# Performance work log

Measured on AMD Instinct MI355X. Metric: run time of the kernel, lower is better.

Reference implementation:

```python
import jax, jax.numpy as jnp
import numpy as np

EPS = 1e-15

def _sqn(x):
    return jnp.sum(x * x, axis=-1, keepdims=True)

def _nrm(x):
    return jnp.sqrt(jnp.clip(_sqn(x), EPS))

def artanh(x):
    return jnp.arctanh(jnp.clip(x, -1 + 1e-7, 1 - 1e-7))

def project(x):
    n = _nrm(x)
    mx = 1.0 - 1e-5
    return jnp.where(n > mx, x / n * mx, x)

def mobius_add(x, y):
    x2, y2 = _sqn(x), _sqn(y)
    xy = jnp.sum(x * y, -1, keepdims=True)
    num = (1 + 2 * xy + y2) * x + (1 - x2) * y
    den = 1 + 2 * xy + x2 * y2
    return num / jnp.clip(den, EPS)

def expmap0(u):
    n = _nrm(u)
    return project(jnp.tanh(n) * u / n)

def logmap0(x):
    n = _nrm(x)
    return artanh(n) * x / n

def pdist(x, y):
    return 2.0 * artanh(_nrm(mobius_add(-x, y)))[..., 0]

def mobius_matvec(x, W):
    # x [..., din], W [din, dout]
    xn = _nrm(x)
    mx = x @ W
    mxn = _nrm(mx)
    return project(jnp.tanh(mxn / xn * artanh(xn)) * mx / mxn)

def mobius_pw_mul(w, x):
    xn = _nrm(x)
    wx = w * x
    wxn = _nrm(wx)
    return project(jnp.tanh(wxn / xn * artanh(xn)) * wx / wxn)

def mobius_linear(x, W, b, nonlin=None):
    out = project(mobius_add(mobius_matvec(x, W), b))
    if nonlin is not None:
        out = project(expmap0(nonlin(logmap0(out))))
    return out

def poincare_to_klein(x):
    return 2 * x / (1 + _sqn(x))

def klein_to_poincare(k):
    return k / (1 + jnp.sqrt(jnp.clip(1 - _sqn(k), EPS)))

def weighted_mobius_midpoint(values, weights):
    # values [..., L, d], weights [..., L, 1]; gyromidpoint via Klein model
    kl = poincare_to_klein(values)
    gamma = 1.0 / jnp.sqrt(jnp.clip(1 - _sqn(kl), EPS))
    num = jnp.sum(weights * gamma * kl, axis=-2)
    den = jnp.sum(weights * gamma, axis=-2)
    return klein_to_poincare(num / jnp.clip(den, EPS))

def mobius_gru(x_seq, Wih, Whh, bias):
    # x_seq [L,B,din]; Wih [3H,din]; Whh [3H,H]; bias [3,H] (points on ball)
    H = Whh.shape[1]
    W_ir, W_ihh, W_iz = jnp.split(Wih, 3, axis=0)
    W_hr, W_hhh, W_hz = jnp.split(Whh, 3, axis=0)
    b_r, b_h, b_z = bias[0], bias[1], bias[2]
    def one_tf(W, h, U, x, b):
        return mobius_add(mobius_add(mobius_matvec(h, W.T), mobius_matvec(x, U.T)), b)
    def step(h, x):
        z = jax.nn.sigmoid(logmap0(one_tf(W_hz, h, W_iz, x, b_z)))
        r = jax.nn.sigmoid(logmap0(one_tf(W_hr, h, W_ir, x, b_r)))
        rh = mobius_pw_mul(r, h)
        h_tilde = one_tf(W_hhh, rh, W_ihh, x, b_h)
        delta = mobius_add(-h, h_tilde)
        hn = mobius_add(h, mobius_pw_mul(z, delta))
        return hn, hn
    h0 = jnp.zeros((x_seq.shape[1], H), x_seq.dtype)
    return jax.lax.scan(step, h0, x_seq)[1]  # [L,B,H]

def mobius_rnn(x_seq, W, U, b):
    # x_seq [L,B,d]; W [d,d] hidden->hidden, U [d,d] input->hidden
    def step(h, x):
        hn = project(mobius_add(mobius_add(mobius_matvec(h, W), mobius_matvec(x, U)), b))
        return hn, hn
    h0 = jnp.zeros(x_seq.shape[1:], x_seq.dtype)
    return jax.lax.scan(step, h0, x_seq)[1]

def distance_attention(values, pos_idx, pos_embeds, Wq, bq, Wk, bk, beta):
    # values [B,L,d], pos_idx [B,L] int
    pe = pos_embeds[pos_idx]
    attn_emb = mobius_add(values, pe)
    q = mobius_linear(attn_emb, Wq, bq)
    k = mobius_linear(attn_emb, Wk, bk)
    d = pdist(q, k)                      # [B,L]
    w = jax.nn.softmax(-beta * d, axis=1)
    return weighted_mobius_midpoint(values, w[..., None]), w

def _forward(context, ctx_position, mentions, mention_chars,
             word_lut, char_lut,
             gru_f_Wih, gru_f_Whh, gru_f_b, gru_b_Wih, gru_b_Whh, gru_b_b,
             w2s_W, w2s_b,
             men_pos, men_Wq, men_bq, men_Wk, men_bk, men_beta,
             char_W, char_U, char_b,
             cc_Wa, cc_Wb, cc_bias,
             ctx_pos, ctx_Wq, ctx_bq, ctx_Wk, ctx_bk, ctx_beta,
             fc_Wm, fc_Wc, fc_Wch, fc_bias,
             mlr_p, mlr_a):
    # ---- mention encoder ----
    men_emb = word_lut[mentions]                                   # B x ML x E
    mv = mobius_linear(men_emb, w2s_W, w2s_b, nonlin=jnp.tanh)     # B x ML x 2S
    ML = mentions.shape[1]
    pos_idx = jnp.where(mentions > 0, jnp.arange(1, ML + 1)[None, :], 0)
    mention_vec, _ = distance_attention(mv, pos_idx, men_pos, men_Wq, men_bq, men_Wk, men_bk, men_beta)
    ch = char_lut[mention_chars]                                   # B x CL x S
    char_states = mobius_rnn(ch.transpose(1, 0, 2), char_W, char_U, char_b).transpose(1, 0, 2)
    char_vec = weighted_mobius_midpoint(char_states, jnp.ones_like(char_states[..., :1]))
    # ---- context encoder (bi-directional hyperbolic GRU) ----
    fwd_emb = word_lut[context].transpose(1, 0, 2)                 # L x B x E
    bkwd_emb = word_lut[context[:, ::-1]].transpose(1, 0, 2)
    fwd_states = mobius_gru(fwd_emb, gru_f_Wih, gru_f_Whh, gru_f_b).transpose(1, 0, 2)
    bkwd_states = mobius_gru(bkwd_emb, gru_b_Wih, gru_b_Whh, gru_b_b).transpose(1, 0, 2)[:, ::-1]
    # ---- mobius concat of directions ----
    ctx = project(mobius_add(mobius_add(mobius_matvec(fwd_states, cc_Wa), mobius_matvec(bkwd_states, cc_Wb)), cc_bias))
    ctx_vec, _ = distance_attention(ctx, ctx_position, ctx_pos, ctx_Wq, ctx_bq, ctx_Wk, ctx_bk, ctx_beta)
    # ---- full mobius concat ----
    joint = mobius_add(mobius_matvec(mention_vec, fc_Wm), mobius_matvec(ctx_vec, fc_Wc))
    joint = project(mobius_add(mobius_add(joint, mobius_matvec(char_vec, fc_Wch)), fc_bias))
    # ---- hyperbolic MLR ----
    z = mobius_add(-mlr_p[None], joint[:, None])                   # B x C x D
    a_n = jnp.sqrt(jnp.clip(jnp.sum(mlr_a * mlr_a, -1), EPS))      # C
    num = 2 * jnp.einsum('bcd,cd->bc', z, mlr_a)
    den = jnp.clip(1 - jnp.sum(z * z, -1), EPS) * a_n
    return 2 * a_n * jnp.arcsinh(num / den)                        # B x C

def setup_inputs() -> dict:
    key = jax.random.key(0)
    ks = iter(jax.random.split(key, 64))
    B, L, ML, CL = 256, 128, 8, 16
    V, CV, E, S, C = 50000, 128, 300, 256, 128
    S2, D = 2 * 256, 5 * 256
    POS_CTX = 2 * 64 + 2  # context_len*2+2
    def u(k, shape, a):
        return jax.random.uniform(k, shape, jnp.float32, -a, a)
    def ball(k, shape, a=1e-4):
        return expmap0(u(k, shape, a))
    def wmat(k, din, dout):
        return u(k, (din, dout), 1.0 / np.sqrt(din))
    inp = {}
    inp['context'] = jax.random.randint(next(ks), (B, L), 0, V)
    inp['ctx_position'] = jax.random.randint(next(ks), (B, L), 0, POS_CTX)
    inp['mentions'] = jax.random.randint(next(ks), (B, ML), 0, V)
    inp['mention_chars'] = jax.random.randint(next(ks), (B, CL), 0, CV)
    inp['word_lut'] = ball(next(ks), (V, E))
    inp['char_lut'] = ball(next(ks), (CV, S))
    for pre in ('gru_f', 'gru_b'):
        inp[pre + '_Wih'] = u(next(ks), (3 * S, E), 1.0 / np.sqrt(S))
        inp[pre + '_Whh'] = u(next(ks), (3 * S, S), 1.0 / np.sqrt(S))
        inp[pre + '_b'] = ball(next(ks), (3, S))
    inp['w2s_W'] = wmat(next(ks), E, S2)
    inp['w2s_b'] = ball(next(ks), (S2,))
    inp['men_pos'] = ball(next(ks), (ML + 1, S2))
    inp['men_Wq'] = wmat(next(ks), S2, S2)
    inp['men_bq'] = ball(next(ks), (S2,))
    inp['men_Wk'] = wmat(next(ks), S2, S2)
    inp['men_bk'] = ball(next(ks), (S2,))
    inp['men_beta'] = u(next(ks), (1,), 0.01)
    inp['char_W'] = wmat(next(ks), S, S)
    inp['char_U'] = wmat(next(ks), S, S)
    inp['char_b'] = ball(next(ks), (S,))
    inp['cc_Wa'] = wmat(next(ks), S, S2)
    inp['cc_Wb'] = wmat(next(ks), S, S2)
    inp['cc_bias'] = ball(next(ks), (S2,))
    inp['ctx_pos'] = ball(next(ks), (POS_CTX, S2))
    inp['ctx_Wq'] = wmat(next(ks), S2, S2)
    inp['ctx_bq'] = ball(next(ks), (S2,))
    inp['ctx_Wk'] = wmat(next(ks), S2, S2)
    inp['ctx_bk'] = ball(next(ks), (S2,))
    inp['ctx_beta'] = u(next(ks), (1,), 0.01)
    inp['fc_Wm'] = wmat(next(ks), S2, D)
    inp['fc_Wc'] = wmat(next(ks), S2, D)
    inp['fc_Wch'] = wmat(next(ks), S, D)
    inp['fc_bias'] = ball(next(ks), (D,))
    inp['mlr_p'] = ball(next(ks), (C, D))
    inp['mlr_a'] = u(next(ks), (C, D), 1.0 / np.sqrt(D))
    return inp

def reference(context, ctx_position, mentions, mention_chars,
              word_lut, char_lut,
              gru_f_Wih, gru_f_Whh, gru_f_b, gru_b_Wih, gru_b_Whh, gru_b_b,
              w2s_W, w2s_b,
              men_pos, men_Wq, men_bq, men_Wk, men_bk, men_beta,
              char_W, char_U, char_b,
              cc_Wa, cc_Wb, cc_bias,
              ctx_pos, ctx_Wq, ctx_bq, ctx_Wk, ctx_bk, ctx_beta,
              fc_Wm, fc_Wc, fc_Wch, fc_bias,
              mlr_p, mlr_a):
    return _forward(context, ctx_position, mentions, mention_chars,
                    word_lut, char_lut,
                    gru_f_Wih, gru_f_Whh, gru_f_b, gru_b_Wih, gru_b_Whh, gru_b_b,
                    w2s_W, w2s_b,
                    men_pos, men_Wq, men_bq, men_Wk, men_bk, men_beta,
                    char_W, char_U, char_b,
                    cc_Wa, cc_Wb, cc_bias,
                    ctx_pos, ctx_Wq, ctx_bq, ctx_Wk, ctx_bk, ctx_beta,
                    fc_Wm, fc_Wc, fc_Wch, fc_bias,
                    mlr_p, mlr_a)
```

## Files before the change

### kernel.cpp

```cpp
#include <hip/hip_runtime.h>
#include <cstddef>
#include <cstdint>


#define EPS_  1e-15f
#define PMAX_ 0.99999f

typedef __attribute__((ext_vector_type(8))) short bf16x8;
typedef __attribute__((ext_vector_type(4))) float f32x4;
typedef __attribute__((ext_vector_type(8))) unsigned short us8;

__device__ __forceinline__ float wred(float v){
#pragma unroll
  for (int o = 32; o; o >>= 1) v += __shfl_xor(v, o, 64);
  return v;
}
__device__ __forceinline__ void wred2(float& a, float& b){
#pragma unroll
  for (int o = 32; o; o >>= 1){ a += __shfl_xor(a, o, 64); b += __shfl_xor(b, o, 64); }
}
__device__ __forceinline__ void wred3(float& a, float& b, float& c){
#pragma unroll
  for (int o = 32; o; o >>= 1){
    a += __shfl_xor(a, o, 64); b += __shfl_xor(b, o, 64); c += __shfl_xor(c, o, 64);
  }
}
__device__ __forceinline__ void wred4(float& a, float& b, float& c, float& d){
#pragma unroll
  for (int o = 32; o; o >>= 1){
    a += __shfl_xor(a, o, 64); b += __shfl_xor(b, o, 64);
    c += __shfl_xor(c, o, 64); d += __shfl_xor(d, o, 64);
  }
}
__device__ __forceinline__ float wredmax(float v){
#pragma unroll
  for (int o = 32; o; o >>= 1) v = fmaxf(v, __shfl_xor(v, o, 64));
  return v;
}
__device__ __forceinline__ float snorm(float s){ return sqrtf(fmaxf(s, EPS_)); }
__device__ __forceinline__ float clamp11(float x){
  return fminf(fmaxf(x, -1.f + 1e-7f), 1.f - 1e-7f);
}
__device__ __forceinline__ float bf2f(unsigned short u){
  union { unsigned int i; float f; } v; v.i = ((unsigned int)u) << 16; return v.f;
}
__device__ __forceinline__ unsigned short f2bf(float f){
  union { float f; unsigned int i; } v; v.f = f;
  unsigned int x = v.i;
  x += 0x7fffu + ((x >> 16) & 1u);
  return (unsigned short)(x >> 16);
}
__device__ __forceinline__ float bflo(unsigned u){
  union { unsigned i; float f; } v; v.i = u << 16; return v.f;
}
__device__ __forceinline__ float bfhi(unsigned u){
  union { unsigned i; float f; } v; v.i = u & 0xffff0000u; return v.f;
}

template<int N>
__device__ __forceinline__ float sq_part(const float* a){
  float s = 0.f;
#pragma unroll
  for (int i = 0; i < N; i++) s += a[i]*a[i];
  return s;
}
template<int N>
__device__ __forceinline__ float dot_part(const float* a, const float* b){
  float s = 0.f;
#pragma unroll
  for (int i = 0; i < N; i++) s += a[i]*b[i];
  return s;
}
template<int N>
__device__ __forceinline__ void madd_vec(const float* x, float x2, const float* y,
                                         float y2, float xy, float* o){
  const float c1 = 1.f + 2.f*xy + y2;
  const float c2 = 1.f - x2;
  const float inv = 1.f / fmaxf(1.f + 2.f*xy + x2*y2, EPS_);
#pragma unroll
  for (int i = 0; i < N; i++) o[i] = (c1*x[i] + c2*y[i]) * inv;
}
template<int N>
__device__ __forceinline__ void mt_project(float* v, float mxn2, float xn2, float* n2out){
  const float xn  = snorm(xn2);
  const float mxn = snorm(mxn2);
  const float t   = tanhf(mxn/xn * atanhf(clamp11(xn)));
  float sc = t/mxn;
  float n2 = sc*sc*mxn2;
  const float n = snorm(n2);
  if (n > PMAX_){ const float s = PMAX_/n; sc *= s; n2 *= s*s; }
#pragma unroll
  for (int i = 0; i < N; i++) v[i] *= sc;
  *n2out = n2;
// ... 165 lines not shown
      if (kb < K){
        const float4 f = *reinterpret_cast<const float4*>(Bm + (long)kb*N + n0 + bn);
        bv[0]=f.x; bv[1]=f.y; bv[2]=f.z; bv[3]=f.w;
      } else { bv[0]=bv[1]=bv[2]=bv[3]=0.f; }
    }
    __syncthreads();
    As[sk+0][sm]=av[0]; As[sk+1][sm]=av[1]; As[sk+2][sm]=av[2]; As[sk+3][sm]=av[3];
    *reinterpret_cast<float4*>(&Bs[bk][bn]) = make_float4(bv[0],bv[1],bv[2],bv[3]);
    __syncthreads();
#pragma unroll
    for (int k = 0; k < 8; k++){
      float a[8], bb[8];
      *(float4*)&a[0]  = *(const float4*)&As[k][tr*8];
      *(float4*)&a[4]  = *(const float4*)&As[k][tr*8+4];
      *(float4*)&bb[0] = *(const float4*)&Bs[k][tc*8];
      *(float4*)&bb[4] = *(const float4*)&Bs[k][tc*8+4];
#pragma unroll
      for (int i = 0; i < 8; i++)
#pragma unroll
        for (int j = 0; j < 8; j++) acc[i][j] += a[i]*bb[j];
    }
  }
#pragma unroll
  for (int i = 0; i < 8; i++){
    const long row = m0 + tr*8 + i;
    *(float4*)(Cm + row*N + n0 + tc*8)     = make_float4(acc[i][0],acc[i][1],acc[i][2],acc[i][3]);
    *(float4*)(Cm + row*N + n0 + tc*8 + 4) = make_float4(acc[i][4],acc[i][5],acc[i][6],acc[i][7]);
  }
}

__global__ __launch_bounds__(256) void transpose_k(const float* __restrict__ src,
    float* __restrict__ dst, int R, int Kc)
{
  __shared__ float t[32][33];
  const int bx = blockIdx.x * 32;
  const int by = blockIdx.y * 32;
  const int tx = threadIdx.x & 31, ty = threadIdx.x >> 5;
#pragma unroll
  for (int i = 0; i < 32; i += 8){
    const int j = by + ty + i, k = bx + tx;
    t[ty+i][tx] = (j < R && k < Kc) ? src[(long)j*Kc + k] : 0.f;
  }
  __syncthreads();
#pragma unroll
  for (int i = 0; i < 32; i += 8){
    const int k = bx + ty + i, j = by + tx;
    if (k < Kc && j < R) dst[(long)k*R + j] = t[tx][ty+i];
  }
}

__global__ __launch_bounds__(256) void packT16(const float* __restrict__ src,
    unsigned short* __restrict__ dst, int K, int N, int Kp)
{
  __shared__ float t[32][33];
  const int bx = blockIdx.x*32;
  const int by = blockIdx.y*32;
  const int tx = threadIdx.x & 31, ty = threadIdx.x >> 5;
#pragma unroll
  for (int i = 0; i < 32; i += 8){
    const int k = bx + ty + i, n = by + tx;
    t[ty+i][tx] = (k < K && n < N) ? src[(long)k*N + n] : 0.f;
  }
  __syncthreads();
#pragma unroll
  for (int i = 0; i < 32; i += 8){
    const int k = bx + tx, n = by + ty + i;
    if (k < Kp && n < N) dst[(long)n*Kp + k] = f2bf(t[tx][ty+i]);
  }
}

__global__ void pack_wih(const float* __restrict__ w0, const float* __restrict__ w1,
                         unsigned short* __restrict__ dst)
{
  const int tid = blockIdx.x*256 + threadIdx.x;
  if (tid < 2*768*320){
    const int d = tid / (768*320);
    const int rem = tid - d*768*320;
    const int n = rem / 320, k = rem - n*320;
    const float* src = d ? w1 : w0;
    dst[tid] = (k < 300) ? f2bf(src[n*300 + k]) : (unsigned short)0;
  }
}

__global__ void pack_whh16(const float* __restrict__ WtHH,
                           unsigned short* __restrict__ Wrz16,
                           unsigned short* __restrict__ Wh16)
{
  const int tid = blockIdx.x*256 + threadIdx.x;
  if (tid < 2*256*768){
    const int col = tid % 768, rk = tid / 768;
    const unsigned short v = f2bf(WtHH[tid]);
    if (col < 256)       Wrz16[(long)rk*512 + col] = v;
    else if (col < 512)  Wh16 [(long)rk*256 + (col - 256)] = v;
    else                 Wrz16[(long)rk*512 + 256 + (col - 512)] = v;
  }
}

__global__ void build_idx(const int* __restrict__ context, const int* __restrict__ mchars,
                          int* __restrict__ ctxidx, int* __restrict__ chidx)
{
  const int tid = blockIdx.x*256 + threadIdx.x;
  if (tid < 32768){
    const int t = tid >> 8, b = tid & 255;
    ctxidx[tid] = context[b*128 + t];
  } else if (tid < 32768 + 4096){
    const int o = tid - 32768;
    const int t = o >> 8, b = o & 255;
    chidx[o] = mchars[b*16 + t];
  }
}

__global__ __launch_bounds__(256) void sqn_gather(const float* __restrict__ lut,
    const int* __restrict__ idx, int K, float* __restrict__ outp)
{
  const int wv = threadIdx.x >> 6, lane = threadIdx.x & 63;
  const int r = blockIdx.x*4 + wv;
  const float* row = lut + (long)idx[r]*K;
  float s = 0.f;
  for (int k = lane; k < K; k += 64) s += row[k]*row[k];
  s = wred(s);
  if (lane == 0) outp[r] = s;
}

__global__ __launch_bounds__(256) void xg_transform(const float* __restrict__ mx,
    const float* __restrict__ xsqn, unsigned short* __restrict__ outp,
    float* __restrict__ n2o, int G)
{
  const int wv = threadIdx.x >> 6, lane = threadIdx.x & 63;
  const int wg = blockIdx.x*4 + wv;
  const int row = wg / G, g = wg - row*G;
  const long base = (long)row*(G*256) + g*256;
  float M[4];
#pragma unroll
  for (int i = 0; i < 4; i++) M[i] = mx[base + i*64 + lane];
  const float mxn2 = wred(sq_part<4>(M));
  float pn2; mt_project<4>(M, mxn2, xsqn[row], &pn2);
  float s = 0.f;
#pragma unroll
  for (int i = 0; i < 4; i++){
    const unsigned short u = f2bf(M[i]);
    outp[base + i*64 + lane] = u;
    const float rv = bf2f(u);
    s += rv*rv;
  }
  s = wred(s);
  if (lane == 0) n2o[wg] = s;
}

#define GRU_LDS_BYTES 153664

__global__ __launch_bounds__(512,1) void gru_kernel(
    const unsigned short* __restrict__ xg,
    const float* __restrict__ xgn2,
    const unsigned short* __restrict__ Wrz16,
    const unsigned short* __restrict__ Wh16,
    const float* __restrict__ bias_f, const float* __restrict__ bias_b,
    unsigned short* __restrict__ states_f, unsigned short* __restrict__ states_b)
{
  extern __shared__ __align__(16) char smem[];
  float* wbuf = (float*)smem;
  float* hs   = (float*)(smem + 131072);
  float* part = (float*)(smem + 133120);
  float* rhb  = (float*)(smem + 149504);
  float* zb   = (float*)(smem + 151552);
  float* scal = (float*)(smem + 153600);

  const int bid = blockIdx.x;
  const int dir = bid >> 7;
  const int brow0 = (bid & 127) * 2;
  const int tid = threadIdx.x;
  const int w = tid >> 6, lane = tid & 63;
  const int j0 = lane << 2;

  const unsigned short* xgd = xg + (long)dir*32768*768;
  const float* xnd = xgn2 + (long)dir*32768*3;
  const unsigned short* wrz_d = Wrz16 + (long)dir*256*512;
  const unsigned short* wh_d  = Wh16  + (long)dir*256*256;
  const float* bias = dir ? bias_b : bias_f;
  unsigned short* states = dir ? states_b : states_f;

  const int fg  = w & 1;
  const int kq4 = w >> 1;
  const int qk8 = w;
  const int crow  = (w >> 1) & 1;
  const int cgate = w & 1;

  float bg[4], bh4[4] = {0,0,0,0};
  float bg2, bh2 = 0.f;
#pragma unroll
  for (int i = 0; i < 4; i++) bg[i] = bias[(cgate ? 512 : 0) + j0 + i];
  bg2 = wred(sq_part<4>(bg));
  if (w < 2){
#pragma unroll
    for (int i = 0; i < 4; i++) bh4[i] = bias[256 + j0 + i];
    bh2 = wred(sq_part<4>(bh4));
  }

  float h[4] = {0.f,0.f,0.f,0.f};
  float hn2 = 0.f;
  if (w < 2){
#pragma unroll
    for (int i = 0; i < 4; i++) hs[w*256 + j0 + i] = 0.f;
    if (lane == 0){ scal[w*2 + 0] = 0.f; scal[w*2 + 1] = 0.f; }
  }

  int cb = 0;
  stage64k8(wrz_d, wbuf, w, lane);

  for (int t = 0; t < 128; t++){
    const int tt = dir ? (127 - t) : t;
    float xgv[4] = {0,0,0,0}, y2g = 0.f, xgh4[4] = {0,0,0,0}, y2h = 0.f;
    if (w < 4){
      const long rxg = (long)tt*256 + brow0 + crow;
      const ushort4 u = *(const ushort4*)(xgd + rxg*768 + (cgate ? 512 : 0) + j0);
      xgv[0]=bf2f(u.x); xgv[1]=bf2f(u.y); xgv[2]=bf2f(u.z); xgv[3]=bf2f(u.w);
      y2g = xnd[rxg*3 + (cgate ? 2 : 0)];
      if (w < 2){
        const long rxh = (long)tt*256 + brow0 + w;
        const ushort4 uh = *(const ushort4*)(xgd + rxh*768 + 256 + j0);
        xgh4[0]=bf2f(uh.x); xgh4[1]=bf2f(uh.y); xgh4[2]=bf2f(uh.z); xgh4[3]=bf2f(uh.w);
        y2h = xnd[rxh*3 + 1];
      }
    }

    float s00=0.f,s01=0.f,s02=0.f,s03=0.f, s10=0.f,s11=0.f,s12=0.f,s13=0.f;
#pragma unroll 1
    for (int c = 0; c < 4; c++){
      __syncthreads();
      if (c < 3) stage64k8((const char*)wrz_d + (size_t)(c+1)*65536,
                           wbuf + (cb^1)*16384, w, lane);
      const uint2* wb2 = (const uint2*)(wbuf + cb*16384);
      const int kb = c*64 + kq4*16;
#pragma unroll
      for (int kk = 0; kk < 4; kk++){
        const float4 hb0 = *(const float4*)&hs[0*256 + kb + kk*4];
        const float4 hb1 = *(const float4*)&hs[1*256 + kb + kk*4];
#pragma unroll
        for (int q = 0; q < 4; q++){
          const uint2 wvv = wb2[(kq4*16 + kk*4 + q)*128 + fg*64 + lane];
          const float w0 = bflo(wvv.x), w1 = bfhi(wvv.x);
          const float w2 = bflo(wvv.y), w3 = bfhi(wvv.y);
          const float h0 = (&hb0.x)[q], h1 = (&hb1.x)[q];
          s00 += h0*w0; s01 += h0*w1; s02 += h0*w2; s03 += h0*w3;
          s10 += h1*w0; s11 += h1*w1; s12 += h1*w2; s13 += h1*w3;
        }
      }
      cb ^= 1;
    }
    {
      float* p1 = part + kq4*1024 + fg*256 + j0;
      *(float4*)p1         = make_float4(s00,s01,s02,s03);
      *(float4*)(p1 + 512) = make_float4(s10,s11,s12,s13);
    }
    __syncthreads();
    stage64k8(wh_d, wbuf + (cb^1)*16384, w, lane);
    cb ^= 1;

    if (w < 4){
      const float* pa = part + crow*512 + cgate*256 + j0;
      const float4 a0 = *(const float4*)pa;
      const float4 a1 = *(const float4*)(pa + 1024);
      const float4 a2 = *(const float4*)(pa + 2048);
      const float4 a3 = *(const float4*)(pa + 3072);
      float a[4] = { (a0.x+a1.x)+(a2.x+a3.x), (a0.y+a1.y)+(a2.y+a3.y),
                     (a0.z+a1.z)+(a2.z+a3.z), (a0.w+a1.w)+(a2.w+a3.w) };
      const float hn2v = scal[crow*2 + 0];
      const float xn_h = snorm(hn2v), art_h = atanhf(clamp11(xn_h));
      const float p2 = wred(sq_part<4>(a));
      float sc, n2; mt_scale(p2, xn_h, art_h, &sc, &n2);
#pragma unroll
      for (int i = 0; i < 4; i++) a[i] *= sc;
      const float xy = wred(dot_part<4>(a, xgv));
      float m1[4]; madd_vec<4>(a, n2, xgv, y2g, xy, m1);
      float m1n2 = sq_part<4>(m1), xyb = dot_part<4>(m1, bg);
      wred2(m1n2, xyb);
      float m2[4]; madd_vec<4>(m1, m1n2, bg, bg2, xyb, m2);
      const float m2n2 = wred(sq_part<4>(m2));
      const float nn = snorm(m2n2), fgc = atanhf(clamp11(nn))/nn;
      float g4[4];
#pragma unroll
      for (int i = 0; i < 4; i++) g4[i] = 1.f/(1.f + expf(-fgc*m2[i]));
      if (cgate == 0){
        float h4[4];
        *(float4*)h4 = *(const float4*)&hs[crow*256 + j0];
        float rh[4]; float wx2 = 0.f;
#pragma unroll
        for (int i = 0; i < 4; i++){ rh[i] = g4[i]*h4[i]; wx2 += rh[i]*rh[i]; }
        wx2 = wred(wx2);
        float rhn2, scrh;
        {
          const float wxn = snorm(wx2);
          const float trh = tanhf(wxn/xn_h * art_h);
          scrh = trh/wxn; rhn2 = trh*trh;
          const float n = snorm(rhn2);
          if (n > PMAX_){ const float f = PMAX_/n; scrh *= f; rhn2 *= f*f; }
        }
#pragma unroll
        for (int i = 0; i < 4; i++) rh[i] *= scrh;
        *(float4*)&rhb[crow*256 + j0] = make_float4(rh[0],rh[1],rh[2],rh[3]);
        if (lane == 0) scal[crow*2 + 1] = rhn2;
      } else {
        *(float4*)&zb[crow*256 + j0] = make_float4(g4[0],g4[1],g4[2],g4[3]);
      }
    }

    float r00=0.f,r01=0.f,r02=0.f,r03=0.f, r10=0.f,r11=0.f,r12=0.f,r13=0.f;
#pragma unroll 1
    for (int c = 0; c < 2; c++){
      __syncthreads();
      if (c < 1) stage64k8((const char*)wh_d + 65536, wbuf + (cb^1)*16384, w, lane);
      const uint2* wb2 = (const uint2*)(wbuf + cb*16384);
      const int kb = c*128 + qk8*16;
#pragma unroll
      for (int kk = 0; kk < 4; kk++){
        const float4 hb0 = *(const float4*)&rhb[0*256 + kb + kk*4];
        const float4 hb1 = *(const float4*)&rhb[1*256 + kb + kk*4];
#pragma unroll
        for (int q = 0; q < 4; q++){
          const uint2 wvv = wb2[(qk8*16 + kk*4 + q)*64 + lane];
          const float w0 = bflo(wvv.x), w1 = bfhi(wvv.x);
          const float w2 = bflo(wvv.y), w3 = bfhi(wvv.y);
          const float h0 = (&hb0.x)[q], h1 = (&hb1.x)[q];
          r00 += h0*w0; r01 += h0*w1; r02 += h0*w2; r03 += h0*w3;
          r10 += h1*w0; r11 += h1*w1; r12 += h1*w2; r13 += h1*w3;
        }
      }
      cb ^= 1;
    }
    {
      float* p2 = part + qk8*512 + j0;
      *(float4*)p2         = make_float4(r00,r01,r02,r03);
      *(float4*)(p2 + 256) = make_float4(r10,r11,r12,r13);
    }
    __syncthreads();
    if (t < 127){
      stage64k8(wrz_d, wbuf + (cb^1)*16384, w, lane);
      cb ^= 1;
    }

    if (w < 2){
      float ah[4];
      {
        float4 p[8];
#pragma unroll
        for (int q = 0; q < 8; q++)
          p[q] = *(const float4*)(part + q*512 + w*256 + j0);
        ah[0] = ((p[0].x+p[1].x)+(p[2].x+p[3].x)) + ((p[4].x+p[5].x)+(p[6].x+p[7].x));
        ah[1] = ((p[0].y+p[1].y)+(p[2].y+p[3].y)) + ((p[4].y+p[5].y)+(p[6].y+p[7].y));
        ah[2] = ((p[0].z+p[1].z)+(p[2].z+p[3].z)) + ((p[4].z+p[5].z)+(p[6].z+p[7].z));
        ah[3] = ((p[0].w+p[1].w)+(p[2].w+p[3].w)) + ((p[4].w+p[5].w)+(p[6].w+p[7].w));
      }
      const float rhn2v = scal[w*2 + 1];
      const float rxn = snorm(rhn2v), artr = atanhf(clamp11(rxn));
      float mx2 = sq_part<4>(ah), xyraw = dot_part<4>(ah, xgh4);
      wred2(mx2, xyraw);
      float sch, pn2; mt_scale(mx2, rxn, artr, &sch, &pn2);
#pragma unroll
      for (int i = 0; i < 4; i++) ah[i] *= sch;
      const float xy = xyraw * sch;
      float m1[4]; madd_vec<4>(ah, pn2, xgh4, y2h, xy, m1);
      float m1n2 = sq_part<4>(m1), xyb = dot_part<4>(m1, bh4);
      wred2(m1n2, xyb);
      float ht[4]; madd_vec<4>(m1, m1n2, bh4, bh2, xyb, ht);
      float htn2 = sq_part<4>(ht);
      float nh[4];
#pragma unroll
      for (int i = 0; i < 4; i++) nh[i] = -h[i];
      float xyd = dot_part<4>(nh, ht);
      wred2(htn2, xyd);
      float dl[4]; madd_vec<4>(nh, hn2, ht, htn2, xyd, dl);
      float z4[4];
      *(float4*)z4 = *(const float4*)&zb[w*256 + j0];
      float pw[4]; float dln2 = 0.f, wz2 = 0.f, xyhr = 0.f;
#pragma unroll
      for (int i = 0; i < 4; i++){
        dln2 += dl[i]*dl[i];
        pw[i] = z4[i]*dl[i];
        wz2  += pw[i]*pw[i];
        xyhr += h[i]*pw[i];
      }
      wred3(dln2, wz2, xyhr);
      float pwn2, scpw;
      {
        const float dn   = snorm(dln2);
        const float artd = atanhf(clamp11(dn));
        const float wzn  = snorm(wz2);
        const float tpw  = tanhf(wzn/dn * artd);
        scpw = tpw/wzn; pwn2 = tpw*tpw;
        const float n = snorm(pwn2);
        if (n > PMAX_){ const float f = PMAX_/n; scpw *= f; pwn2 *= f*f; }
      }
#pragma unroll
      for (int i = 0; i < 4; i++) pw[i] *= scpw;
      const float xyh = xyhr * scpw;
      float hnew[4]; madd_vec<4>(h, hn2, pw, pwn2, xyh, hnew);
#pragma unroll
      for (int i = 0; i < 4; i++) h[i] = hnew[i];
      hn2 = wred(sq_part<4>(h));
      *(float4*)&hs[w*256 + j0] = make_float4(h[0],h[1],h[2],h[3]);
      if (lane == 0) scal[w*2 + 0] = hn2;
      unsigned short* srow = states + ((long)(brow0 + w)*128 + tt)*256 + j0;
      ushort4 su; su.x=f2bf(h[0]); su.y=f2bf(h[1]); su.z=f2bf(h[2]); su.w=f2bf(h[3]);
      *(ushort4*)srow = su;
    }
  }
}

__global__ __launch_bounds__(256) void char_rnn(
    const unsigned short* __restrict__ xgc,
    const float* __restrict__ Wc,
    const float* __restrict__ cb,
    float* __restrict__ cstates)
{
  const int wv = threadIdx.x >> 6, lane = threadIdx.x & 63;
  const int b = blockIdx.x*4 + wv;
  const int j0 = lane << 2;
  __shared__ __align__(16) float hs[4][256];
  float h[4] = {0.f,0.f,0.f,0.f};
  float hn2 = 0.f;
#pragma unroll
  for (int i = 0; i < 4; i++) hs[wv][j0+i] = 0.f;
  float cbv[4];
#pragma unroll
  for (int i = 0; i < 4; i++) cbv[i] = cb[j0+i];
  const float cb2 = wred(sq_part<4>(cbv));
  for (int t = 0; t < 16; t++){
    __syncthreads();
    const unsigned short* xr = xgc + ((long)t*256 + b)*256;
    float xgv[4];
    { const ushort4 u = *(const ushort4*)(xr + j0); xgv[0]=bf2f(u.x); xgv[1]=bf2f(u.y); xgv[2]=bf2f(u.z); xgv[3]=bf2f(u.w); }
    float a[4]={0.f,0.f,0.f,0.f};
#pragma unroll 2
    for (int k0 = 0; k0 < 256; k0 += 4){
      const float4 hk = *(const float4*)&hs[wv][k0];
#pragma unroll
      for (int kk = 0; kk < 4; kk++){
        const float hv = (&hk.x)[kk];
        const float4 w4 = *(const float4*)(Wc + (long)(k0+kk)*256 + j0);
        a[0] += hv*w4.x; a[1] += hv*w4.y; a[2] += hv*w4.z; a[3] += hv*w4.w;
      }
    }
    const float mxn2 = wred(sq_part<4>(a));
    float pn2; mt_project<4>(a, mxn2, hn2, &pn2);
    const float y2 = wred(sq_part<4>(xgv));
    const float xy = wred(dot_part<4>(a, xgv));
    float m1[4]; madd_vec<4>(a, pn2, xgv, y2, xy, m1);
    const float m1n2 = wred(sq_part<4>(m1));
    const float xyb  = wred(dot_part<4>(m1, cbv));
    float m2[4]; madd_vec<4>(m1, m1n2, cbv, cb2, xyb, m2);
    float m2n2 = wred(sq_part<4>(m2));
    project_vec<4>(m2, &m2n2);
#pragma unroll
    for (int i = 0; i < 4; i++) h[i] = m2[i];
    hn2 = m2n2;
    *(float4*)&hs[wv][j0] = make_float4(h[0],h[1],h[2],h[3]);
    *(float4*)(cstates + ((long)b*16 + t)*256 + j0) = make_float4(h[0],h[1],h[2],h[3]);
  }
}

__global__ __launch_bounds__(256) void cc_rowwise(const unsigned short* __restrict__ sf,
    const unsigned short* __restrict__ sb, const float* __restrict__ mxa,
    const float* __restrict__ mxb, const float* __restrict__ ccb,
    unsigned short* __restrict__ ctxo, int rowoff)
{
  const int wv = threadIdx.x >> 6, lane = threadIdx.x & 63;
  const int rloc = blockIdx.x*4 + wv;
  const long r = rowoff + rloc;
  float s = 0.f;
#pragma unroll
  for (int i = 0; i < 4; i++){ const float v = bf2f(sf[r*256 + i*64+lane]); s += v*v; }
  const float sfn2 = wred(s);
  s = 0.f;
#pragma unroll
  for (int i = 0; i < 4; i++){ const float v = bf2f(sb[r*256 + i*64+lane]); s += v*v; }
  const float sbn2 = wred(s);
  float A[8], Bv[8];
#pragma unroll
  for (int i = 0; i < 8; i++){ A[i]  = mxa[(long)rloc*512 + i*64+lane];
                               Bv[i] = mxb[(long)rloc*512 + i*64+lane]; }
  float pan2, pbn2;
  { const float n2 = wred(sq_part<8>(A));  mt_project<8>(A,  n2, sfn2, &pan2); }
  { const float n2 = wred(sq_part<8>(Bv)); mt_project<8>(Bv, n2, sbn2, &pbn2); }
// ... 332 lines not shown

__global__ __launch_bounds__(256) void mlr_kernel(const float* __restrict__ joint,
    const float* __restrict__ P, const float* __restrict__ A, float* __restrict__ outp)
{
  const int wv = threadIdx.x >> 6, lane = threadIdx.x & 63;
  const int pair = blockIdx.x*4 + wv;
  const long b = pair >> 7, c = pair & 127;
  float Pv[20], J[20];
#pragma unroll
  for (int i = 0; i < 20; i++){
    Pv[i] = -P[c*1280 + i*64+lane];
    J[i]  = joint[b*1280 + i*64+lane];
  }
  const float p2 = wred(sq_part<20>(Pv));
  const float j2 = wred(sq_part<20>(J));
  const float xy = wred(dot_part<20>(Pv, J));
  float Z[20]; madd_vec<20>(Pv, p2, J, j2, xy, Z);
  float sza = 0.f, sz2 = 0.f, sa2 = 0.f;
#pragma unroll
  for (int i = 0; i < 20; i++){
    const float a = A[c*1280 + i*64+lane];
    sza += Z[i]*a; sz2 += Z[i]*Z[i]; sa2 += a*a;
  }
  float za = sza, z2 = sz2, a2 = sa2;
  wred3(za, z2, a2);
  const float an = sqrtf(fmaxf(a2, EPS_));
  const float v = 2.f*za / (fmaxf(1.f - z2, EPS_)*an);
  if (lane == 0) outp[pair] = 2.f*an*asinhf(v);
}

extern "C" void kernel_launch(void* const* d_in, const int* in_sizes, int n_in,
                              void* d_out, int out_size, void* d_ws, size_t ws_size,
                              hipStream_t stream)
{
  (void)in_sizes; (void)n_in; (void)out_size;
  const int*   context   = (const int*)  d_in[0];
  const int*   ctx_position=(const int*) d_in[1];
  const int*   mentions  = (const int*)  d_in[2];
  const int*   mchars    = (const int*)  d_in[3];
  const float* word_lut  = (const float*)d_in[4];
  const float* char_lut  = (const float*)d_in[5];
  const float* gf_Wih    = (const float*)d_in[6];
  const float* gf_Whh    = (const float*)d_in[7];
  const float* gf_b      = (const float*)d_in[8];
  const float* gb_Wih    = (const float*)d_in[9];
  const float* gb_Whh    = (const float*)d_in[10];
  const float* gb_b      = (const float*)d_in[11];
  const float* w2s_W     = (const float*)d_in[12];
  const float* w2s_b     = (const float*)d_in[13];
  const float* men_pos   = (const float*)d_in[14];
  const float* men_Wq    = (const float*)d_in[15];
  const float* men_bq    = (const float*)d_in[16];
  const float* men_Wk    = (const float*)d_in[17];
  const float* men_bk    = (const float*)d_in[18];
  const float* men_beta  = (const float*)d_in[19];
  const float* char_W    = (const float*)d_in[20];
  const float* char_U    = (const float*)d_in[21];
  const float* char_b    = (const float*)d_in[22];
  const float* cc_Wa     = (const float*)d_in[23];
  const float* cc_Wb     = (const float*)d_in[24];
  const float* cc_bias   = (const float*)d_in[25];
  const float* ctx_pos_t = (const float*)d_in[26];
  const float* ctx_Wq    = (const float*)d_in[27];
  const float* ctx_bq    = (const float*)d_in[28];
  const float* ctx_Wk    = (const float*)d_in[29];
  const float* ctx_bk    = (const float*)d_in[30];
  const float* ctx_beta  = (const float*)d_in[31];
  const float* fc_Wm     = (const float*)d_in[32];
  const float* fc_Wc     = (const float*)d_in[33];
  const float* fc_Wch    = (const float*)d_in[34];
  const float* fc_bias   = (const float*)d_in[35];
  const float* mlr_p     = (const float*)d_in[36];
  const float* mlr_a     = (const float*)d_in[37];
  float* out = (float*)d_out;

  char* wsb = (char*)d_ws;
  size_t off = 0;
  auto alloc = [&](size_t bytes) -> void* {
    void* p = wsb + off;
    off += (bytes + 255) & ~(size_t)255;
    return p;
  };
  float* WtHH = (float*)alloc(2UL*256*768*4);
  unsigned short* Wrz16 = (unsigned short*)alloc(2UL*256*512*2);
  unsigned short* Wh16  = (unsigned short*)alloc(2UL*256*256*2);
  unsigned short* WihP  = (unsigned short*)alloc(2UL*768*320*2);
  unsigned short* ctxWqP= (unsigned short*)alloc(512UL*512*2);
  unsigned short* ctxWkP= (unsigned short*)alloc(512UL*512*2);
  unsigned short* ccWaP = (unsigned short*)alloc(512UL*256*2);
  unsigned short* ccWbP = (unsigned short*)alloc(512UL*256*2);
  unsigned short* menWqP= (unsigned short*)alloc(512UL*512*2);
  unsigned short* menWkP= (unsigned short*)alloc(512UL*512*2);
  unsigned short* w2sP  = (unsigned short*)alloc(512UL*320*2);
  unsigned short* charUP= (unsigned short*)alloc(256UL*256*2);
  int*   ctxidx = (int*)alloc(32768UL*4);
  int*   chidx  = (int*)alloc(4096UL*4);
  float* xsqn   = (float*)alloc(32768UL*4);
  float* msqn   = (float*)alloc(2048UL*4);
  float* chsqn  = (float*)alloc(4096UL*4);
  unsigned short* xg = (unsigned short*)alloc(2UL*32768*768*2);
  float* xgn2 = (float*)alloc(2UL*32768*3*4);
  float* chn2d = (float*)alloc(4096UL*4);
  unsigned short* states_f = (unsigned short*)alloc(32768UL*256*2);
  unsigned short* states_b = (unsigned short*)alloc(32768UL*256*2);
  unsigned short* ctxv = (unsigned short*)alloc(32768UL*512*2);
  float* attn_sqn = (float*)alloc(32768UL*4);
  float* dctx = (float*)alloc(32768UL*4);
  float* wctx = (float*)alloc(32768UL*4);
  float* ctx_vec = (float*)alloc(256UL*512*4);
  float* mxbuf = (float*)alloc(2UL*8192*512*4);
  float* mv = (float*)alloc(2048UL*512*4);
  unsigned short* attn_embm = (unsigned short*)alloc(2048UL*512*2);
  float* amsqn = (float*)alloc(2048UL*4);
  float* dm = (float*)alloc(2048UL*4);
  float* wm = (float*)alloc(2048UL*4);
  float* mention_vec = (float*)alloc(256UL*512*4);
  unsigned short* xgc = (unsigned short*)alloc(4096UL*256*2);
  float* char_states = (float*)alloc(4096UL*256*4);
  float* char_vec = (float*)alloc(256UL*256*4);
  float* joint = (float*)alloc(256UL*1280*4);
  if (off > ws_size) return;
  unsigned short* attn_embc = xg;
  float* mxh0 = mxbuf;
  float* mxh1 = mxbuf + 8192UL*512;

  transpose_k<<<dim3(8,24), 256,0,stream>>>(gf_Whh, WtHH,            768, 256);
  transpose_k<<<dim3(8,24), 256,0,stream>>>(gb_Whh, WtHH + 256*768,  768, 256);
  pack_whh16<<<1536,256,0,stream>>>(WtHH, Wrz16, Wh16);
  pack_wih<<<1920,256,0,stream>>>(gf_Wih, gb_Wih, WihP);
  packT16<<<dim3(16,16),256,0,stream>>>(ctx_Wq, ctxWqP, 512, 512, 512);
  packT16<<<dim3(16,16),256,0,stream>>>(ctx_Wk, ctxWkP, 512, 512, 512);
  packT16<<<dim3(8,16), 256,0,stream>>>(cc_Wa,  ccWaP,  256, 512, 256);
  packT16<<<dim3(8,16), 256,0,stream>>>(cc_Wb,  ccWbP,  256, 512, 256);
  packT16<<<dim3(16,16),256,0,stream>>>(men_Wq, menWqP, 512, 512, 512);
  packT16<<<dim3(16,16),256,0,stream>>>(men_Wk, menWkP, 512, 512, 512);
  packT16<<<dim3(10,16),256,0,stream>>>(w2s_W,  w2sP,   300, 512, 320);
  packT16<<<dim3(8,8),  256,0,stream>>>(char_U, charUP, 256, 256, 256);

  build_idx<<<144,256,0,stream>>>(context, mchars, ctxidx, chidx);
  sqn_gather<<<8192,256,0,stream>>>(word_lut, ctxidx, 300, xsqn);
  sqn_gather<<<512, 256,0,stream>>>(word_lut, mentions, 300, msqn);
  sqn_gather<<<1024,256,0,stream>>>(char_lut, chidx, 256, chsqn);

  for (int d2 = 0; d2 < 2; d2++){
    const unsigned short* wihp = WihP + (size_t)d2*768*320;
    for (int c = 0; c < 4; c++){
      mfma_mm<1><<<dim3(6,128),256,0,stream>>>(word_lut, ctxidx + c*8192, wihp,
                                               mxbuf, 8192, 768, 300, 320);
      xg_transform<<<6144,256,0,stream>>>(mxbuf, xsqn + c*8192,
          xg + ((size_t)d2*32768 + (size_t)c*8192)*768,
          xgn2 + ((size_t)d2*32768 + (size_t)c*8192)*3, 3);
    }
  }

  (void)hipFuncSetAttribute((const void*)gru_kernel,
      hipFuncAttributeMaxDynamicSharedMemorySize, GRU_LDS_BYTES);
  gru_kernel<<<256,512,GRU_LDS_BYTES,stream>>>(xg, xgn2, Wrz16, Wh16,
                                               gf_b, gb_b, states_f, states_b);

  for (int c = 0; c < 4; c++){
    mfma_mm<2><<<dim3(4,128),256,0,stream>>>(states_f + (size_t)c*8192*256, nullptr,
                                             ccWaP, mxh0, 8192, 512, 256, 256);
    mfma_mm<2><<<dim3(4,128),256,0,stream>>>(states_b + (size_t)c*8192*256, nullptr,
                                             ccWbP, mxh1, 8192, 512, 256, 256);
    cc_rowwise<<<2048,256,0,stream>>>(states_f, states_b, mxh0, mxh1, cc_bias,
                                      ctxv, c*8192);
  }

  attn_add<<<8192,256,0,stream>>>(ctxv, ctx_position, ctx_pos_t, attn_embc, attn_sqn);
  for (int c = 0; c < 4; c++){
    mfma_mm<2><<<dim3(4,128),256,0,stream>>>(attn_embc + (size_t)c*8192*512, nullptr,
                                             ctxWqP, mxh0, 8192, 512, 512, 512);
    mfma_mm<2><<<dim3(4,128),256,0,stream>>>(attn_embc + (size_t)c*8192*512, nullptr,
                                             ctxWkP, mxh1, 8192, 512, 512, 512);
    qk_pdist<<<2048,256,0,stream>>>(mxh0, mxh1, attn_sqn + c*8192, ctx_bq, ctx_bk,
                                    dctx + c*8192);
  }
  softmax128<<<64,256,0,stream>>>(dctx, ctx_beta, wctx);
  midpoint_wide<<<256,512,0,stream>>>(ctxv, wctx, ctx_vec);

  mfma_mm<1><<<dim3(4,32),256,0,stream>>>(word_lut, mentions, w2sP, mxh0,
                                          2048, 512, 300, 320);
  mv_rowwise<<<512,256,0,stream>>>(mxh0, msqn, w2s_b, mv);
  attn_add_m<<<512,256,0,stream>>>(mv, mentions, men_pos, attn_embm, amsqn);
  mfma_mm<2><<<dim3(4,32),256,0,stream>>>(attn_embm, nullptr, menWqP, mxh0,
                                          2048, 512, 512, 512);
  mfma_mm<2><<<dim3(4,32),256,0,stream>>>(attn_embm, nullptr, menWkP, mxh1,
                                          2048, 512, 512, 512);
  qk_pdist<<<512,256,0,stream>>>(mxh0, mxh1, amsqn, men_bq, men_bk, dm);
  softmax8<<<1,256,0,stream>>>(dm, men_beta, wm);
  midpoint_kernel<8,false,true><<<64,256,0,stream>>>(mv, wm, mention_vec, 8);

  mfma_mm<1><<<dim3(2,64),256,0,stream>>>(char_lut, chidx, charUP, mxh0,
                                          4096, 256, 256, 256);
  xg_transform<<<1024,256,0,stream>>>(mxh0, chsqn, xgc, chn2d, 1);
  char_rnn<<<64,256,0,stream>>>(xgc, char_W, char_b, char_states);
  midpoint_kernel<4,false,false><<<64,256,0,stream>>>(char_states, nullptr, char_vec, 16);

  float* jm = mxh0;
  float* jc = mxh0 + 256UL*1280;
  float* jch = mxh0 + 2UL*256*1280;
  mm_kernel<0><<<dim3(10,2),256,0,stream>>>(mention_vec, nullptr, fc_Wm, jm, 256, 1280, 512);
  mm_kernel<0><<<dim3(10,2),256,0,stream>>>(ctx_vec,     nullptr, fc_Wc, jc, 256, 1280, 512);
  mm_kernel<0><<<dim3(10,2),256,0,stream>>>(char_vec,    nullptr, fc_Wch, jch, 256, 1280, 256);
  final_rowwise<<<64,256,0,stream>>>(jm, jc, jch, mention_vec, ctx_vec, char_vec,
                                     fc_bias, joint);
  mlr_kernel<<<8192,256,0,stream>>>(joint, mlr_p, mlr_a, out);
}
```

Baseline: 2.737 ms.

## Switch GRU recurrent matvec to packed fp16 with fdot2 accumulation

The recurrent weights are repacked as fp16 pairs along K instead of bf16 pairs along N, and the hidden and reset-scaled states are stored in LDS as packed half2. The inner matvec loops then use v_dot2 (fdot2) instructions, replacing bf16-to-float unpacking and scalar FMAs, which roughly halves the ALU instruction count per step of the serial GRU. This trades some precision (fp16 range and rounding for both weights and hidden state) for fewer instructions, and changes the LDS layout and access pattern.

```diff
diff --git a/kernel.cpp b/kernel.cpp
--- a/kernel.cpp
+++ b/kernel.cpp
@@ -9,6 +9,20 @@
 typedef __attribute__((ext_vector_type(8))) short bf16x8;
 typedef __attribute__((ext_vector_type(4))) float f32x4;
 typedef __attribute__((ext_vector_type(8))) unsigned short us8;
+typedef _Float16 half2_t __attribute__((ext_vector_type(2)));
+
+__device__ __forceinline__ half2_t as_h2(unsigned u){
+  union { unsigned u; half2_t h; } v; v.u = u; return v.h;
+}
+__device__ __forceinline__ unsigned packh2(float a, float b){
+  union { half2_t h; unsigned u; } v;
+  v.h[0] = (_Float16)a; v.h[1] = (_Float16)b; return v.u;
+}
+#if __has_builtin(__builtin_amdgcn_fdot2)
+#define FDOT2(a,b,c) __builtin_amdgcn_fdot2((a),(b),(c),false)
+#else
+#define FDOT2(a,b,c) ((c) + (float)(a)[0]*(float)(b)[0] + (float)(a)[1]*(float)(b)[1])
+#endif
 
 __device__ __forceinline__ float wred(float v){
 #pragma unroll
@@ -340,17 +354,20 @@
   }
 }
 
-__global__ void pack_whh16(const float* __restrict__ WtHH,
-                           unsigned short* __restrict__ Wrz16,
-                           unsigned short* __restrict__ Wh16)
+__global__ void pack_whh_f16(const float* __restrict__ WtHH,
+                             unsigned* __restrict__ Wrz2,
+                             unsigned* __restrict__ Wh2)
 {
   const int tid = blockIdx.x*256 + threadIdx.x;
-  if (tid < 2*256*768){
-    const int col = tid % 768, rk = tid / 768;
-    const unsigned short v = f2bf(WtHH[tid]);
-    if (col < 256)       Wrz16[(long)rk*512 + col] = v;
-    else if (col < 512)  Wh16 [(long)rk*256 + (col - 256)] = v;
-    else                 Wrz16[(long)rk*512 + 256 + (col - 512)] = v;
+  if (tid < 2*128*768){
+    const int col = tid % 768;
+    const int rest = tid / 768;
+    const int kp = rest & 127, dir = rest >> 7;
+    const float* s0 = WtHH + ((long)(dir*256 + 2*kp))*768 + col;
+    const unsigned u = packh2(s0[0], s0[768]);
+    if (col < 256)       Wrz2[(long)(dir*128 + kp)*512 + col] = u;
+    else if (col < 512)  Wh2 [(long)(dir*128 + kp)*256 + (col - 256)] = u;
+    else                 Wrz2[(long)(dir*128 + kp)*512 + 256 + (col - 512)] = u;
   }
 }
 
@@ -405,23 +422,23 @@
   if (lane == 0) n2o[wg] = s;
 }
 
-#define GRU_LDS_BYTES 153664
+#define GRU_LDS_BYTES 151808
 
 __global__ __launch_bounds__(512,1) void gru_kernel(
     const unsigned short* __restrict__ xg,
     const float* __restrict__ xgn2,
-    const unsigned short* __restrict__ Wrz16,
-    const unsigned short* __restrict__ Wh16,
+    const unsigned* __restrict__ Wrz2,
+    const unsigned* __restrict__ Wh2,
     const float* __restrict__ bias_f, const float* __restrict__ bias_b,
     unsigned short* __restrict__ states_f, unsigned short* __restrict__ states_b)
 {
   extern __shared__ __align__(16) char smem[];
-  float* wbuf = (float*)smem;
-  float* hs   = (float*)(smem + 131072);
-  float* part = (float*)(smem + 133120);
-  float* rhb  = (float*)(smem + 149504);
-  float* zb   = (float*)(smem + 151552);
-  float* scal = (float*)(smem + 153600);
+  float*    wbuf = (float*)smem;
+  unsigned* hsp  = (unsigned*)(smem + 131072);
+  unsigned* rhp  = (unsigned*)(smem + 132096);
+  float*    part = (float*)(smem + 133120);
+  float*    zb   = (float*)(smem + 149504);
+  float*    scal = (float*)(smem + 151552);
 
   const int bid = blockIdx.x;
   const int dir = bid >> 7;
@@ -432,8 +449,8 @@
 
   const unsigned short* xgd = xg + (long)dir*32768*768;
   const float* xnd = xgn2 + (long)dir*32768*3;
-  const unsigned short* wrz_d = Wrz16 + (long)dir*256*512;
-  const unsigned short* wh_d  = Wh16  + (long)dir*256*256;
+  const unsigned* wrz_d = Wrz2 + (long)dir*128*512;
+  const unsigned* wh_d  = Wh2  + (long)dir*128*256;
   const float* bias = dir ? bias_b : bias_f;
   unsigned short* states = dir ? states_b : states_f;
 
@@ -457,8 +474,8 @@
   float h[4] = {0.f,0.f,0.f,0.f};
   float hn2 = 0.f;
   if (w < 2){
-#pragma unroll
-    for (int i = 0; i < 4; i++) hs[w*256 + j0 + i] = 0.f;
+    hsp[w*128 + lane*2]     = 0u;
+    hsp[w*128 + lane*2 + 1] = 0u;
     if (lane == 0){ scal[w*2 + 0] = 0.f; scal[w*2 + 1] = 0.f; }
   }
 
@@ -487,21 +504,22 @@
       __syncthreads();
       if (c < 3) stage64k8((const char*)wrz_d + (size_t)(c+1)*65536,
                            wbuf + (cb^1)*16384, w, lane);
-      const uint2* wb2 = (const uint2*)(wbuf + cb*16384);
-      const int kb = c*64 + kq4*16;
-#pragma unroll
-      for (int kk = 0; kk < 4; kk++){
-        const float4 hb0 = *(const float4*)&hs[0*256 + kb + kk*4];
-        const float4 hb1 = *(const float4*)&hs[1*256 + kb + kk*4];
-#pragma unroll
-        for (int q = 0; q < 4; q++){
-          const uint2 wvv = wb2[(kq4*16 + kk*4 + q)*128 + fg*64 + lane];
-          const float w0 = bflo(wvv.x), w1 = bfhi(wvv.x);
-          const float w2 = bflo(wvv.y), w3 = bfhi(wvv.y);
-          const float h0 = (&hb0.x)[q], h1 = (&hb1.x)[q];
-          s00 += h0*w0; s01 += h0*w1; s02 += h0*w2; s03 += h0*w3;
-          s10 += h1*w0; s11 += h1*w1; s12 += h1*w2; s13 += h1*w3;
-        }
+      const unsigned* wb = (const unsigned*)(wbuf + cb*16384);
+      const int kpg = c*32;
+#pragma unroll
+      for (int kp8 = 0; kp8 < 8; kp8++){
+        const int kpl = kq4*8 + kp8;
+        const half2_t h0 = as_h2(hsp[kpg + kpl]);
+        const half2_t h1 = as_h2(hsp[128 + kpg + kpl]);
+        const uint4 wq = *(const uint4*)&wb[kpl*512 + fg*256 + j0];
+        s00 = FDOT2(as_h2(wq.x), h0, s00);
+        s01 = FDOT2(as_h2(wq.y), h0, s01);
+        s02 = FDOT2(as_h2(wq.z), h0, s02);
+        s03 = FDOT2(as_h2(wq.w), h0, s03);
+        s10 = FDOT2(as_h2(wq.x), h1, s10);
+        s11 = FDOT2(as_h2(wq.y), h1, s11);
+        s12 = FDOT2(as_h2(wq.z), h1, s12);
+        s13 = FDOT2(as_h2(wq.w), h1, s13);
       }
       cb ^= 1;
     }
@@ -540,7 +558,12 @@
       for (int i = 0; i < 4; i++) g4[i] = 1.f/(1.f + expf(-fgc*m2[i]));
       if (cgate == 0){
         float h4[4];
-        *(float4*)h4 = *(const float4*)&hs[crow*256 + j0];
+        {
+          const half2_t pa0 = as_h2(hsp[crow*128 + lane*2]);
+          const half2_t pa1 = as_h2(hsp[crow*128 + lane*2 + 1]);
+          h4[0] = (float)pa0[0]; h4[1] = (float)pa0[1];
+          h4[2] = (float)pa1[0]; h4[3] = (float)pa1[1];
+        }
         float rh[4]; float wx2 = 0.f;
 #pragma unroll
         for (int i = 0; i < 4; i++){ rh[i] = g4[i]*h4[i]; wx2 += rh[i]*rh[i]; }
@@ -555,7 +578,8 @@
         }
 #pragma unroll
         for (int i = 0; i < 4; i++) rh[i] *= scrh;
-        *(float4*)&rhb[crow*256 + j0] = make_float4(rh[0],rh[1],rh[2],rh[3]);
+        rhp[crow*128 + lane*2]     = packh2(rh[0], rh[1]);
+        rhp[crow*128 + lane*2 + 1] = packh2(rh[2], rh[3]);
         if (lane == 0) scal[crow*2 + 1] = rhn2;
       } else {
         *(float4*)&zb[crow*256 + j0] = make_float4(g4[0],g4[1],g4[2],g4[3]);
@@ -567,21 +591,22 @@
     for (int c = 0; c < 2; c++){
       __syncthreads();
       if (c < 1) stage64k8((const char*)wh_d + 65536, wbuf + (cb^1)*16384, w, lane);
-      const uint2* wb2 = (const uint2*)(wbuf + cb*16384);
-      const int kb = c*128 + qk8*16;
-#pragma unroll
-      for (int kk = 0; kk < 4; kk++){
-        const float4 hb0 = *(const float4*)&rhb[0*256 + kb + kk*4];
-        const float4 hb1 = *(const float4*)&rhb[1*256 + kb + kk*4];
-#pragma unroll
-        for (int q = 0; q < 4; q++){
-          const uint2 wvv = wb2[(qk8*16 + kk*4 + q)*64 + lane];
-          const float w0 = bflo(wvv.x), w1 = bfhi(wvv.x);
-          const float w2 = bflo(wvv.y), w3 = bfhi(wvv.y);
-          const float h0 = (&hb0.x)[q], h1 = (&hb1.x)[q];
-          r00 += h0*w0; r01 += h0*w1; r02 += h0*w2; r03 += h0*w3;
-          r10 += h1*w0; r11 += h1*w1; r12 += h1*w2; r13 += h1*w3;
-        }
+      const unsigned* wb = (const unsigned*)(wbuf + cb*16384);
+      const int kpg = c*64;
+#pragma unroll
+      for (int kp8 = 0; kp8 < 8; kp8++){
+        const int kpl = qk8*8 + kp8;
+        const half2_t h0 = as_h2(rhp[kpg + kpl]);
+        const half2_t h1 = as_h2(rhp[128 + kpg + kpl]);
+        const uint4 wq = *(const uint4*)&wb[kpl*256 + j0];
+        r00 = FDOT2(as_h2(wq.x), h0, r00);
+        r01 = FDOT2(as_h2(wq.y), h0, r01);
+        r02 = FDOT2(as_h2(wq.z), h0, r02);
+        r03 = FDOT2(as_h2(wq.w), h0, r03);
+        r10 = FDOT2(as_h2(wq.x), h1, r10);
+        r11 = FDOT2(as_h2(wq.y), h1, r11);
+        r12 = FDOT2(as_h2(wq.z), h1, r12);
+        r13 = FDOT2(as_h2(wq.w), h1, r13);
       }
       cb ^= 1;
     }
@@ -655,7 +680,8 @@
 #pragma unroll
       for (int i = 0; i < 4; i++) h[i] = hnew[i];
       hn2 = wred(sq_part<4>(h));
-      *(float4*)&hs[w*256 + j0] = make_float4(h[0],h[1],h[2],h[3]);
+      hsp[w*128 + lane*2]     = packh2(h[0], h[1]);
+      hsp[w*128 + lane*2 + 1] = packh2(h[2], h[3]);
       if (lane == 0) scal[w*2 + 0] = hn2;
       unsigned short* srow = states + ((long)(brow0 + w)*128 + tt)*256 + j0;
       ushort4 su; su.x=f2bf(h[0]); su.y=f2bf(h[1]); su.z=f2bf(h[2]); su.w=f2bf(h[3]);
@@ -1154,8 +1180,8 @@
     return p;
   };
   float* WtHH = (float*)alloc(2UL*256*768*4);
-  unsigned short* Wrz16 = (unsigned short*)alloc(2UL*256*512*2);
-  unsigned short* Wh16  = (unsigned short*)alloc(2UL*256*256*2);
+  unsigned* Wrz2 = (unsigned*)alloc(2UL*128*512*4);
+  unsigned* Wh2  = (unsigned*)alloc(2UL*128*256*4);
   unsigned short* WihP  = (unsigned short*)alloc(2UL*768*320*2);
   unsigned short* ctxWqP= (unsigned short*)alloc(512UL*512*2);
   unsigned short* ctxWkP= (unsigned short*)alloc(512UL*512*2);
@@ -1198,7 +1224,7 @@
 
   transpose_k<<<dim3(8,24), 256,0,stream>>>(gf_Whh, WtHH,            768, 256);
   transpose_k<<<dim3(8,24), 256,0,stream>>>(gb_Whh, WtHH + 256*768,  768, 256);
-  pack_whh16<<<1536,256,0,stream>>>(WtHH, Wrz16, Wh16);
+  pack_whh_f16<<<768,256,0,stream>>>(WtHH, Wrz2, Wh2);
   pack_wih<<<1920,256,0,stream>>>(gf_Wih, gb_Wih, WihP);
   packT16<<<dim3(16,16),256,0,stream>>>(ctx_Wq, ctxWqP, 512, 512, 512);
   packT16<<<dim3(16,16),256,0,stream>>>(ctx_Wk, ctxWkP, 512, 512, 512);
@@ -1227,7 +1253,7 @@
 
   (void)hipFuncSetAttribute((const void*)gru_kernel,
       hipFuncAttributeMaxDynamicSharedMemorySize, GRU_LDS_BYTES);
-  gru_kernel<<<256,512,GRU_LDS_BYTES,stream>>>(xg, xgn2, Wrz16, Wh16,
+  gru_kernel<<<256,512,GRU_LDS_BYTES,stream>>>(xg, xgn2, Wrz2, Wh2,
                                                gf_b, gb_b, states_f, states_b);
 
   for (int c = 0; c < 4; c++){
```

After: 2.524 ms. -7.8%, faster.
